# Kernel optimization log

Measured on AMD Instinct MI355X. Metric: run time of the kernel, lower is better.

The kernel has to match this reference:

```python
import jax, jax.numpy as jnp
import numpy as np

B, S, D, H, DFF = 2, 2048, 1024, 16, 4096
DK = D // H
EPS = 1e-6


def layer_norm(x, alpha, bias):
    # TF reduce_std is biased std; eps added to std (not variance)
    mean = jnp.mean(x, axis=-1, keepdims=True)
    std = jnp.sqrt(jnp.mean((x - mean) ** 2, axis=-1, keepdims=True))
    return alpha * (x - mean) / (std + EPS) + bias


def setup_inputs() -> dict:
    key = jax.random.key(0)
    ks = jax.random.split(key, 10)
    s = 0.02
    return {
        "x": jax.random.normal(ks[0], (B, S, D), jnp.float32),
        "mask": jnp.ones((B, 1, 1, S), jnp.int32),
        "wq": jax.random.normal(ks[1], (D, D), jnp.float32) * s,
        "wk": jax.random.normal(ks[2], (D, D), jnp.float32) * s,
        "wv": jax.random.normal(ks[3], (D, D), jnp.float32) * s,
        "wo": jax.random.normal(ks[4], (D, D), jnp.float32) * s,
        "w1": jax.random.normal(ks[5], (D, DFF), jnp.float32) * s,
        "b1": jnp.zeros((DFF,), jnp.float32),
        "w2": jax.random.normal(ks[6], (DFF, D), jnp.float32) * s,
        "b2": jnp.zeros((D,), jnp.float32),
        "ln1_a": jnp.ones((D,), jnp.float32),
        "ln1_b": jnp.zeros((D,), jnp.float32),
        "ln2_a": jnp.ones((D,), jnp.float32),
        "ln2_b": jnp.zeros((D,), jnp.float32),
    }


def reference(x, mask, wq, wk, wv, wo, w1, b1, w2, b2, ln1_a, ln1_b, ln2_a, ln2_b):
    # --- residual 1: pre-norm self-attention ---
    xn = layer_norm(x, ln1_a, ln1_b)
    q = (xn @ wq).reshape(B, S, H, DK)
    k = (xn @ wk).reshape(B, S, H, DK)
    v = (xn @ wv).reshape(B, S, H, DK)
    scores = jnp.einsum('bqhd,bkhd->bhqk', q, k) / jnp.sqrt(jnp.float32(DK))
    scores = jnp.where(mask == 0, jnp.float32(-1e9), scores)
    attn = jax.nn.softmax(scores, axis=-1)  # dropout = identity at eval
    ctx = jnp.einsum('bhqk,bkhd->bqhd', attn, v).reshape(B, S, D)
    x = x + ctx @ wo
    # --- residual 2: pre-norm FFN ---
    xn = layer_norm(x, ln2_a, ln2_b)
    ff = jax.nn.relu(xn @ w1 + b1) @ w2 + b2
    return x + ff
```

## Files before the change

kernel.cpp:

```cpp
#include <hip/hip_runtime.h>

#define BATCH 2
#define SEQ   2048
#define DMODEL 1024
#define NHEAD 16
#define DHEAD 64
#define DFF_  4096
#define MROWS (BATCH*SEQ)
#define EPS 1e-6f

typedef unsigned short u16;
typedef unsigned int u32;
typedef __bf16 bf16x8 __attribute__((ext_vector_type(8)));
typedef float  f32x4  __attribute__((ext_vector_type(4)));
typedef u32    u32x2  __attribute__((ext_vector_type(2)));

__device__ __forceinline__ float bf2f(u16 h) {
    union { u32 u; float f; } v; v.u = ((u32)h) << 16; return v.f;
}
__device__ __forceinline__ u16 f2bf(float f) {
    union { float f; u32 u; } v; v.f = f;
    u32 u = v.u;
    u32 r = (u + 0x7fffu + ((u >> 16) & 1u)) >> 16;
    return (u16)r;
}

__device__ __forceinline__ void async16(const u16* g, u16* l) {
    __builtin_amdgcn_global_load_lds((const __attribute__((address_space(1))) void*)g,
                                     (__attribute__((address_space(3))) void*)l,
                                     16, 0, 0);
}

__global__ __launch_bounds__(256) void transpose_cvt(const float* __restrict__ in,
                                                     u16* __restrict__ out,
                                                     int R, int C) {
    __shared__ float tile[32][33];
    int c0 = blockIdx.x * 32, r0 = blockIdx.y * 32;
    int x = threadIdx.x, y = threadIdx.y;
    #pragma unroll
    for (int i = 0; i < 32; i += 8)
        tile[y + i][x] = in[(size_t)(r0 + y + i) * C + c0 + x];
    __syncthreads();
    #pragma unroll
    for (int i = 0; i < 32; i += 8)
        out[(size_t)(c0 + y + i) * R + r0 + x] = f2bf(tile[x][y + i]);
}

__global__ __launch_bounds__(256) void transpose_v(const u16* __restrict__ qkv,
                                                   u16* __restrict__ vt) {
    __shared__ u16 tile[32][33];
    int bh = blockIdx.z; int b = bh >> 4, h = bh & 15;
    int k0 = blockIdx.x * 32, d0 = blockIdx.y * 32;
    const u16* in = qkv + ((size_t)(b * SEQ)) * 3072 + 2 * DMODEL + h * DHEAD;
    u16* out = vt + ((size_t)bh * DHEAD) * SEQ;
    int x = threadIdx.x, y = threadIdx.y;
    #pragma unroll
    for (int i = 0; i < 32; i += 8)
        tile[y + i][x] = in[(size_t)(k0 + y + i) * 3072 + d0 + x];
    __syncthreads();
    #pragma unroll
    for (int i = 0; i < 32; i += 8)
        out[(size_t)(d0 + y + i) * SEQ + k0 + x] = tile[x][y + i];
}

__global__ __launch_bounds__(256) void ln_kernel(const float* __restrict__ x,
                                                 const float* __restrict__ alpha,
                                                 const float* __restrict__ beta,
                                                 u16* __restrict__ out) {
    int row = blockIdx.x;
    int t = threadIdx.x;
    const float* xr = x + (size_t)row * DMODEL;
    float4 xv = ((const float4*)xr)[t];
    float f0 = xv.x, f1 = xv.y, f2 = xv.z, f3 = xv.w;
    float s1 = f0 + f1 + f2 + f3;
    float s2 = f0*f0 + f1*f1 + f2*f2 + f3*f3;
    #pragma unroll
    for (int off = 32; off >= 1; off >>= 1) {
        s1 += __shfl_xor(s1, off);
        s2 += __shfl_xor(s2, off);
    }
    __shared__ float r1[4], r2[4];
    int w = t >> 6, lane = t & 63;
    if (lane == 0) { r1[w] = s1; r2[w] = s2; }
    __syncthreads();
    s1 = r1[0] + r1[1] + r1[2] + r1[3];
    s2 = r2[0] + r2[1] + r2[2] + r2[3];
    float mean = s1 * (1.0f / DMODEL);
    float var  = s2 * (1.0f / DMODEL) - mean * mean;
    var = fmaxf(var, 0.0f);
    float inv = 1.0f / (sqrtf(var) + EPS);
    float4 av = ((const float4*)alpha)[t];
    float4 bv = ((const float4*)beta)[t];
    ushort4 ov;
    ov.x = f2bf(av.x * (f0 - mean) * inv + bv.x);
    ov.y = f2bf(av.y * (f1 - mean) * inv + bv.y);
    ov.z = f2bf(av.z * (f2 - mean) * inv + bv.z);
    ov.w = f2bf(av.w * (f3 - mean) * inv + bv.w);
    ((ushort4*)(out + (size_t)row * DMODEL))[t] = ov;
}

#define BK 64

template <int AI, int AJ, bool OUT_F32>
__global__ __launch_bounds__(256) void gemm_bt(const u16* __restrict__ A,
                                               const u16* __restrict__ BT,
                                               void* __restrict__ Cp,
                                               const float* __restrict__ bias,
                                               const float* __restrict__ residual,
                                               int M, int N, int K, int do_relu) {
    constexpr int BMt = AI * 32, BNt = AJ * 32;
    __shared__ u16 As[BMt * BK];
    __shared__ u16 Bs[BNt * BK];
    int t = threadIdx.x;
    int m0 = blockIdx.y * BMt, n0 = blockIdx.x * BNt;
    int lane = t & 63, w = t >> 6;
    int wr = w >> 1, wc = w & 1;
    int lhi = lane >> 4, llo = lane & 15;
    int sr = lane >> 3, sk = lane & 7;
    int skx = (sk ^ sr) * 8;

    f32x4 acc[AI][AJ] = {};

    const u16* Ab = A  + (size_t)m0 * K + skx;
    const u16* Bb = BT + (size_t)n0 * K + skx;

    for (int k0 = 0; k0 < K; k0 += BK) {
        __syncthreads();
        #pragma unroll
        for (int j = 0; j < AI; j++) {
            int blk = w * AI + j;
            async16(Ab + (size_t)(blk * 8 + sr) * K + k0, &As[blk * 512]);
        }
        #pragma unroll
        for (int j = 0; j < AJ; j++) {
            int blk = w * AJ + j;
            async16(Bb + (size_t)(blk * 8 + sr) * K + k0, &Bs[blk * 512]);
        }
        __syncthreads();
        #pragma unroll
        for (int kk = 0; kk < 2; kk++) {
            int slot = ((kk * 4 + lhi) ^ (llo & 7)) * 8;
            bf16x8 af[AI], bfr[AJ];
            #pragma unroll
            for (int i = 0; i < AI; i++)
                af[i]  = *(const bf16x8*)(&As[(wr * 16 * AI + i * 16 + llo) * 64 + slot]);
            #pragma unroll
            for (int j = 0; j < AJ; j++)
                bfr[j] = *(const bf16x8*)(&Bs[(wc * 16 * AJ + j * 16 + llo) * 64 + slot]);
            #pragma unroll
            for (int i = 0; i < AI; i++)
                #pragma unroll
                for (int j = 0; j < AJ; j++)
                    acc[i][j] = __builtin_amdgcn_mfma_f32_16x16x32_bf16(af[i], bfr[j], acc[i][j], 0, 0, 0);
        }
    }

    #pragma unroll
    for (int i = 0; i < AI; i++) {
        #pragma unroll
        for (int rr = 0; rr < 4; rr++) {
            int row = m0 + wr * 16 * AI + i * 16 + lhi * 4 + rr;
            #pragma unroll
            for (int j = 0; j < AJ; j++) {
                int col = n0 + wc * 16 * AJ + j * 16 + llo;
                float v = acc[i][j][rr];
                if (bias)      v += bias[col];
                if (residual)  v += residual[(size_t)row * N + col];
                if (do_relu)   v = fmaxf(v, 0.0f);
                size_t idx = (size_t)row * N + col;
                if (OUT_F32) ((float*)Cp)[idx] = v;
                else         ((u16*)Cp)[idx]   = f2bf(v);
            }
        }
    }
}

#define PSTR 68
#define SCL 0.18033688f

__global__ __launch_bounds__(256) void flash_attn(const u16* __restrict__ qkv,
                                                  const u16* __restrict__ vt,
                                                  const int* __restrict__ mask,
                                                  u16* __restrict__ ctx) {
    __shared__ u16 QPs[4 * 16 * PSTR];
    __shared__ u16 Ks[64 * 64];
    __shared__ u16 VTs[64 * 64];
    __shared__ int msk[64];

    int t = threadIdx.x;
    int w = t >> 6, lane = t & 63, lhi = lane >> 4, llo = lane & 15;
    int sr = lane >> 3, sk = lane & 7;
    int skx = (sk ^ sr) * 8;
    int q0 = blockIdx.x * 64, h = blockIdx.y, b = blockIdx.z;

    const u16* Qg  = qkv + ((size_t)(b * SEQ + q0)) * 3072 + h * DHEAD;
    const u16* Kg  = qkv + ((size_t)(b * SEQ)) * 3072 + DMODEL + h * DHEAD;
    const u16* VTg = vt + ((size_t)((b * NHEAD + h) * DHEAD)) * SEQ;

    #pragma unroll
    for (int j = 0; j < 4; j++) {
        int row = (w * 4 + j) * 8 + sr;
        async16(Qg + (size_t)row * 3072 + skx, &QPs[(w * 4 + j) * 512]);
    }
    __syncthreads();
    bf16x8 qf[2];
    #pragma unroll
    for (int kk = 0; kk < 2; kk++)
        qf[kk] = *(const bf16x8*)&QPs[(w * 16 + llo) * 64 + ((kk * 4 + lhi) ^ (llo & 7)) * 8];

    u16* Ps = QPs + w * (16 * PSTR);

    float l_part[4] = {0.0f, 0.0f, 0.0f, 0.0f};
    f32x4 o_acc[4] = {};

    for (int kt = 0; kt < SEQ; kt += 64) {
        __syncthreads();
        #pragma unroll
        for (int j = 0; j < 2; j++) {
            int row = (w * 2 + j) * 8 + sr;
            async16(Kg  + (size_t)(kt + row) * 3072 + skx, &Ks[(w * 2 + j) * 512]);
            async16(VTg + (size_t)row * SEQ + kt + skx,    &VTs[(w * 2 + j) * 512]);
        }
        if (t < 64) msk[t] = mask[b * SEQ + kt + t];
        __syncthreads();

        f32x4 s[4] = {};
        #pragma unroll
        for (int kk = 0; kk < 2; kk++) {
            #pragma unroll
            for (int j = 0; j < 4; j++) {
                bf16x8 kf = *(const bf16x8*)&Ks[(j * 16 + llo) * 64 + ((kk * 4 + lhi) ^ (llo & 7)) * 8];
                s[j] = __builtin_amdgcn_mfma_f32_16x16x32_bf16(qf[kk], kf, s[j], 0, 0, 0);
            }
        }
        #pragma unroll
        for (int j = 0; j < 4; j++) {
            if (msk[j * 16 + llo] == 0) {
                #pragma unroll
                for (int rr = 0; rr < 4; rr++) s[j][rr] = -1.0e13f;
            }
        }
        #pragma unroll
        for (int rr = 0; rr < 4; rr++) {
            #pragma unroll
            for (int j = 0; j < 4; j++) {
                float p = __builtin_amdgcn_exp2f(s[j][rr] * SCL);
                l_part[rr] += p;
                union { float f; u32 u; } pu; pu.f = p;
                Ps[(lhi * 4 + rr) * PSTR + j * 16 + llo] = (u16)(pu.u >> 16);
            }
        }
        #pragma unroll
        for (int kk = 0; kk < 2; kk++) {
            union { bf16x8 v; u32x2 d[2]; } pf;
            const u16* pp = &Ps[llo * PSTR + kk * 32 + lhi * 8];
            pf.d[0] = *(const u32x2*)pp;
            pf.d[1] = *(const u32x2*)(pp + 4);
            #pragma unroll
            for (int nb = 0; nb < 4; nb++) {
                bf16x8 vf = *(const bf16x8*)&VTs[(nb * 16 + llo) * 64 + ((kk * 4 + lhi) ^ (llo & 7)) * 8];
                o_acc[nb] = __builtin_amdgcn_mfma_f32_16x16x32_bf16(pf.v, vf, o_acc[nb], 0, 0, 0);
            }
        }
    }

    #pragma unroll
    for (int rr = 0; rr < 4; rr++) {
        float l = l_part[rr];
        #pragma unroll
        for (int off = 1; off <= 8; off <<= 1) l += __shfl_xor(l, off);
        float inv = __builtin_amdgcn_rcpf(l);
        int row = q0 + w * 16 + lhi * 4 + rr;
        #pragma unroll
        for (int nb = 0; nb < 4; nb++) {
            int col = h * DHEAD + nb * 16 + llo;
            ctx[((size_t)(b * SEQ) + row) * DMODEL + col] = f2bf(o_acc[nb][rr] * inv);
        }
    }
}

extern "C" void kernel_launch(void* const* d_in, const int* in_sizes, int n_in,
                              void* d_out, int out_size, void* d_ws, size_t ws_size,
                              hipStream_t stream) {
    (void)in_sizes; (void)n_in; (void)out_size; (void)ws_size;
    const float* x    = (const float*)d_in[0];
    const int* mask   = (const int*)d_in[1];
    const float* wq   = (const float*)d_in[2];
    const float* wk   = (const float*)d_in[3];
    const float* wv   = (const float*)d_in[4];
    const float* wo   = (const float*)d_in[5];
    const float* w1   = (const float*)d_in[6];
    const float* b1   = (const float*)d_in[7];
    const float* w2   = (const float*)d_in[8];
    const float* b2   = (const float*)d_in[9];
    const float* ln1a = (const float*)d_in[10];
    const float* ln1b = (const float*)d_in[11];
    const float* ln2a = (const float*)d_in[12];
    const float* ln2b = (const float*)d_in[13];
    float* out = (float*)d_out;

    char* wsb = (char*)d_ws;
    const size_t MB = 1024 * 1024;
    u16*   wqkvT = (u16*)(wsb + 0);
    u16*   woT   = (u16*)(wsb + 6 * MB);
    u16*   w1T   = (u16*)(wsb + 8 * MB);
    u16*   w2T   = (u16*)(wsb + 16 * MB);
    u16*   xn    = (u16*)(wsb + 24 * MB);
    float* x2    = (float*)(wsb + 32 * MB);
    u16*   vt    = (u16*)(wsb + 32 * MB);
    u16*   ctx   = (u16*)(wsb + 48 * MB);
    u16*   qkv   = (u16*)(wsb + 56 * MB);
    u16*   ff1   = (u16*)(wsb + 56 * MB);

    dim3 tb(32, 8);
    transpose_cvt<<<dim3(DMODEL/32, DMODEL/32), tb, 0, stream>>>(wq, wqkvT,               DMODEL, DMODEL);
    transpose_cvt<<<dim3(DMODEL/32, DMODEL/32), tb, 0, stream>>>(wk, wqkvT + 1024*1024,   DMODEL, DMODEL);
    transpose_cvt<<<dim3(DMODEL/32, DMODEL/32), tb, 0, stream>>>(wv, wqkvT + 2*1024*1024, DMODEL, DMODEL);
    transpose_cvt<<<dim3(DMODEL/32, DMODEL/32), tb, 0, stream>>>(wo, woT,                 DMODEL, DMODEL);
    transpose_cvt<<<dim3(DFF_/32,  DMODEL/32),  tb, 0, stream>>>(w1, w1T,                 DMODEL, DFF_);
    transpose_cvt<<<dim3(DMODEL/32, DFF_/32),   tb, 0, stream>>>(w2, w2T,                 DFF_, DMODEL);

    ln_kernel<<<MROWS, 256, 0, stream>>>(x, ln1a, ln1b, xn);
    gemm_bt<4,4,false><<<dim3(3072/128, MROWS/128), 256, 0, stream>>>(xn, wqkvT, qkv,
                                                                      nullptr, nullptr,
                                                                      MROWS, 3072, DMODEL, 0);
    transpose_v<<<dim3(SEQ/32, DHEAD/32, BATCH*NHEAD), tb, 0, stream>>>(qkv, vt);
    flash_attn<<<dim3(SEQ / 64, NHEAD, BATCH), 256, 0, stream>>>(qkv, vt, mask, ctx);
    gemm_bt<2,2,true><<<dim3(DMODEL/64, MROWS/64), 256, 0, stream>>>(ctx, woT, x2,
                                                                     nullptr, x,
                                                                     MROWS, DMODEL, DMODEL, 0);
    ln_kernel<<<MROWS, 256, 0, stream>>>(x2, ln2a, ln2b, xn);
    gemm_bt<4,4,false><<<dim3(DFF_/128, MROWS/128), 256, 0, stream>>>(xn, w1T, ff1,
                                                                     b1, nullptr,
                                                                     MROWS, DFF_, DMODEL, 1);
    gemm_bt<2,2,true><<<dim3(DMODEL/64, MROWS/64), 256, 0, stream>>>(ff1, w2T, out,
                                                                    b2, x2,
                                                                    MROWS, DMODEL, DFF_, 0);
}
```

Before: 399.2 us.

## Use two-wave attention blocks with 32 query rows per wave and permuted V layout

Flash attention now runs 128-thread blocks where each wave handles 32 query rows, so every K and V fragment read from LDS feeds two MFMAs. The V transpose kernel writes key positions in a permuted order so each lane can store its four P values as one packed 8-byte LDS write instead of scattered 16-bit stores. Masking becomes an additive bias folded into an FMA before exp2, and the V transpose uses 16-byte vector loads and stores. In exchange, each wave needs more registers and there are fewer waves per block for hiding latency.

```diff
diff --git a/kernel.cpp b/kernel.cpp
--- a/kernel.cpp
+++ b/kernel.cpp
@@ -46,21 +46,33 @@
         out[(size_t)(c0 + y + i) * R + r0 + x] = f2bf(tile[x][y + i]);
 }
 
-__global__ __launch_bounds__(256) void transpose_v(const u16* __restrict__ qkv,
-                                                   u16* __restrict__ vt) {
-    __shared__ u16 tile[32][33];
-    int bh = blockIdx.z; int b = bh >> 4, h = bh & 15;
-    int k0 = blockIdx.x * 32, d0 = blockIdx.y * 32;
-    const u16* in = qkv + ((size_t)(b * SEQ)) * 3072 + 2 * DMODEL + h * DHEAD;
-    u16* out = vt + ((size_t)bh * DHEAD) * SEQ;
-    int x = threadIdx.x, y = threadIdx.y;
-    #pragma unroll
-    for (int i = 0; i < 32; i += 8)
-        tile[y + i][x] = in[(size_t)(k0 + y + i) * 3072 + d0 + x];
+__global__ __launch_bounds__(256) void transpose_v_perm(const u16* __restrict__ qkv,
+                                                        u16* __restrict__ vtp) {
+    __shared__ u16 tile[64][72];
+    int kt = blockIdx.x * 64;
+    int bh = blockIdx.y; int b = bh >> 4, h = bh & 15;
+    const u16* in = qkv + ((size_t)(b * SEQ + kt)) * 3072 + 2 * DMODEL + h * DHEAD;
+    u16* out = vtp + ((size_t)bh * DHEAD) * SEQ;
+    int t = threadIdx.x;
+    int r = t >> 3, c8 = (t & 7) * 8;
+    #pragma unroll
+    for (int pass = 0; pass < 2; pass++) {
+        int row = r + pass * 32;
+        uint4 v = *(const uint4*)(in + (size_t)row * 3072 + c8);
+        *(uint4*)&tile[row][c8] = v;
+    }
     __syncthreads();
     #pragma unroll
-    for (int i = 0; i < 32; i += 8)
-        out[(size_t)(d0 + y + i) * SEQ + k0 + x] = tile[x][y + i];
+    for (int pass = 0; pass < 2; pass++) {
+        int d = r + pass * 32;
+        u16 o8[8];
+        #pragma unroll
+        for (int e = 0; e < 8; e++) {
+            int c = c8 + e;
+            o8[e] = tile[(c & 3) * 16 + (c >> 2)][d];
+        }
+        *(uint4*)(out + (size_t)d * SEQ + kt + c8) = *(const uint4*)o8;
+    }
 }
 
 __global__ __launch_bounds__(256) void ln_kernel(const float* __restrict__ x,
@@ -175,106 +187,120 @@
     }
 }
 
-#define PSTR 68
+#define PSTR 72
 #define SCL 0.18033688f
 
-__global__ __launch_bounds__(256) void flash_attn(const u16* __restrict__ qkv,
-                                                  const u16* __restrict__ vt,
+__global__ __launch_bounds__(128) void flash_attn(const u16* __restrict__ qkv,
+                                                  const u16* __restrict__ vtp,
                                                   const int* __restrict__ mask,
                                                   u16* __restrict__ ctx) {
-    __shared__ u16 QPs[4 * 16 * PSTR];
+    __shared__ u16 QPs[2 * 32 * PSTR];
     __shared__ u16 Ks[64 * 64];
     __shared__ u16 VTs[64 * 64];
-    __shared__ int msk[64];
+    __shared__ float mbias[64];
 
     int t = threadIdx.x;
-    int w = t >> 6, lane = t & 63, lhi = lane >> 4, llo = lane & 15;
+    int wv = t >> 6, lane = t & 63, lhi = lane >> 4, llo = lane & 15;
     int sr = lane >> 3, sk = lane & 7;
     int skx = (sk ^ sr) * 8;
     int q0 = blockIdx.x * 64, h = blockIdx.y, b = blockIdx.z;
 
     const u16* Qg  = qkv + ((size_t)(b * SEQ + q0)) * 3072 + h * DHEAD;
     const u16* Kg  = qkv + ((size_t)(b * SEQ)) * 3072 + DMODEL + h * DHEAD;
-    const u16* VTg = vt + ((size_t)((b * NHEAD + h) * DHEAD)) * SEQ;
+    const u16* VTg = vtp + ((size_t)((b * NHEAD + h) * DHEAD)) * SEQ;
 
     #pragma unroll
     for (int j = 0; j < 4; j++) {
-        int row = (w * 4 + j) * 8 + sr;
-        async16(Qg + (size_t)row * 3072 + skx, &QPs[(w * 4 + j) * 512]);
+        int blk = wv * 4 + j;
+        async16(Qg + (size_t)(blk * 8 + sr) * 3072 + skx, &QPs[blk * 512]);
     }
     __syncthreads();
-    bf16x8 qf[2];
-    #pragma unroll
-    for (int kk = 0; kk < 2; kk++)
-        qf[kk] = *(const bf16x8*)&QPs[(w * 16 + llo) * 64 + ((kk * 4 + lhi) ^ (llo & 7)) * 8];
-
-    u16* Ps = QPs + w * (16 * PSTR);
-
-    float l_part[4] = {0.0f, 0.0f, 0.0f, 0.0f};
-    f32x4 o_acc[4] = {};
+    bf16x8 qf[2][2];
+    #pragma unroll
+    for (int mi = 0; mi < 2; mi++)
+        #pragma unroll
+        for (int kk = 0; kk < 2; kk++)
+            qf[mi][kk] = *(const bf16x8*)&QPs[(wv * 32 + mi * 16 + llo) * 64 +
+                                              ((kk * 4 + lhi) ^ (llo & 7)) * 8];
+
+    u16* Ps = QPs + wv * (32 * PSTR);
+
+    float l_part[2][4] = {};
+    f32x4 o_acc[2][4] = {};
 
     for (int kt = 0; kt < SEQ; kt += 64) {
         __syncthreads();
         #pragma unroll
-        for (int j = 0; j < 2; j++) {
-            int row = (w * 2 + j) * 8 + sr;
-            async16(Kg  + (size_t)(kt + row) * 3072 + skx, &Ks[(w * 2 + j) * 512]);
-            async16(VTg + (size_t)row * SEQ + kt + skx,    &VTs[(w * 2 + j) * 512]);
-        }
-        if (t < 64) msk[t] = mask[b * SEQ + kt + t];
+        for (int j = 0; j < 4; j++) {
+            int blk = wv * 4 + j;
+            async16(Kg  + (size_t)(kt + blk * 8 + sr) * 3072 + skx, &Ks[blk * 512]);
+            async16(VTg + (size_t)(blk * 8 + sr) * SEQ + kt + skx,  &VTs[blk * 512]);
+        }
+        if (t < 64) mbias[t] = (mask[b * SEQ + kt + t] == 0) ? -1.0e12f : 0.0f;
         __syncthreads();
 
-        f32x4 s[4] = {};
+        f32x4 s0[4] = {}, s1[4] = {};
         #pragma unroll
         for (int kk = 0; kk < 2; kk++) {
             #pragma unroll
             for (int j = 0; j < 4; j++) {
-                bf16x8 kf = *(const bf16x8*)&Ks[(j * 16 + llo) * 64 + ((kk * 4 + lhi) ^ (llo & 7)) * 8];
-                s[j] = __builtin_amdgcn_mfma_f32_16x16x32_bf16(qf[kk], kf, s[j], 0, 0, 0);
-            }
-        }
-        #pragma unroll
-        for (int j = 0; j < 4; j++) {
-            if (msk[j * 16 + llo] == 0) {
+                bf16x8 kf = *(const bf16x8*)&Ks[(j * 16 + llo) * 64 +
+                                                ((kk * 4 + lhi) ^ (llo & 7)) * 8];
+                s0[j] = __builtin_amdgcn_mfma_f32_16x16x32_bf16(qf[0][kk], kf, s0[j], 0, 0, 0);
+                s1[j] = __builtin_amdgcn_mfma_f32_16x16x32_bf16(qf[1][kk], kf, s1[j], 0, 0, 0);
+            }
+        }
+        float mb[4];
+        #pragma unroll
+        for (int j = 0; j < 4; j++) mb[j] = mbias[j * 16 + llo];
+
+        #pragma unroll
+        for (int mi = 0; mi < 2; mi++) {
+            const f32x4* s = mi ? s1 : s0;
+            #pragma unroll
+            for (int rr = 0; rr < 4; rr++) {
+                u32 pu[4];
                 #pragma unroll
-                for (int rr = 0; rr < 4; rr++) s[j][rr] = -1.0e13f;
-            }
-        }
+                for (int j = 0; j < 4; j++) {
+                    float p = __builtin_amdgcn_exp2f(__builtin_fmaf(s[j][rr], SCL, mb[j]));
+                    l_part[mi][rr] += p;
+                    union { float f; u32 u; } c; c.f = p;
+                    pu[j] = c.u;
+                }
+                u32x2 w;
+                w[0] = (pu[0] >> 16) | (pu[1] & 0xffff0000u);
+                w[1] = (pu[2] >> 16) | (pu[3] & 0xffff0000u);
+                *(u32x2*)&Ps[(mi * 16 + lhi * 4 + rr) * PSTR + llo * 4] = w;
+            }
+        }
+        #pragma unroll
+        for (int kk = 0; kk < 2; kk++) {
+            bf16x8 pf0 = *(const bf16x8*)&Ps[(0 * 16 + llo) * PSTR + kk * 32 + lhi * 8];
+            bf16x8 pf1 = *(const bf16x8*)&Ps[(1 * 16 + llo) * PSTR + kk * 32 + lhi * 8];
+            #pragma unroll
+            for (int nb = 0; nb < 4; nb++) {
+                bf16x8 vf = *(const bf16x8*)&VTs[(nb * 16 + llo) * 64 +
+                                                 ((kk * 4 + lhi) ^ (llo & 7)) * 8];
+                o_acc[0][nb] = __builtin_amdgcn_mfma_f32_16x16x32_bf16(pf0, vf, o_acc[0][nb], 0, 0, 0);
+                o_acc[1][nb] = __builtin_amdgcn_mfma_f32_16x16x32_bf16(pf1, vf, o_acc[1][nb], 0, 0, 0);
+            }
+        }
+    }
+
+    #pragma unroll
+    for (int mi = 0; mi < 2; mi++) {
         #pragma unroll
         for (int rr = 0; rr < 4; rr++) {
-            #pragma unroll
-            for (int j = 0; j < 4; j++) {
-                float p = __builtin_amdgcn_exp2f(s[j][rr] * SCL);
-                l_part[rr] += p;
-                union { float f; u32 u; } pu; pu.f = p;
-                Ps[(lhi * 4 + rr) * PSTR + j * 16 + llo] = (u16)(pu.u >> 16);
-            }
-        }
-        #pragma unroll
-        for (int kk = 0; kk < 2; kk++) {
-            union { bf16x8 v; u32x2 d[2]; } pf;
-            const u16* pp = &Ps[llo * PSTR + kk * 32 + lhi * 8];
-            pf.d[0] = *(const u32x2*)pp;
-            pf.d[1] = *(const u32x2*)(pp + 4);
+            float l = l_part[mi][rr];
+            #pragma unroll
+            for (int off = 1; off <= 8; off <<= 1) l += __shfl_xor(l, off);
+            float inv = __builtin_amdgcn_rcpf(l);
+            int row = q0 + wv * 32 + mi * 16 + lhi * 4 + rr;
             #pragma unroll
             for (int nb = 0; nb < 4; nb++) {
-                bf16x8 vf = *(const bf16x8*)&VTs[(nb * 16 + llo) * 64 + ((kk * 4 + lhi) ^ (llo & 7)) * 8];
-                o_acc[nb] = __builtin_amdgcn_mfma_f32_16x16x32_bf16(pf.v, vf, o_acc[nb], 0, 0, 0);
-            }
-        }
-    }
-
-    #pragma unroll
-    for (int rr = 0; rr < 4; rr++) {
-        float l = l_part[rr];
-        #pragma unroll
-        for (int off = 1; off <= 8; off <<= 1) l += __shfl_xor(l, off);
-        float inv = __builtin_amdgcn_rcpf(l);
-        int row = q0 + w * 16 + lhi * 4 + rr;
-        #pragma unroll
-        for (int nb = 0; nb < 4; nb++) {
-            int col = h * DHEAD + nb * 16 + llo;
-            ctx[((size_t)(b * SEQ) + row) * DMODEL + col] = f2bf(o_acc[nb][rr] * inv);
+                int col = h * DHEAD + nb * 16 + llo;
+                ctx[((size_t)(b * SEQ) + row) * DMODEL + col] = f2bf(o_acc[mi][nb][rr] * inv);
+            }
         }
     }
 }
@@ -307,7 +333,7 @@
     u16*   w2T   = (u16*)(wsb + 16 * MB);
     u16*   xn    = (u16*)(wsb + 24 * MB);
     float* x2    = (float*)(wsb + 32 * MB);
-    u16*   vt    = (u16*)(wsb + 32 * MB);
+    u16*   vtp   = (u16*)(wsb + 32 * MB);
     u16*   ctx   = (u16*)(wsb + 48 * MB);
     u16*   qkv   = (u16*)(wsb + 56 * MB);
     u16*   ff1   = (u16*)(wsb + 56 * MB);
@@ -324,8 +350,8 @@
     gemm_bt<4,4,false><<<dim3(3072/128, MROWS/128), 256, 0, stream>>>(xn, wqkvT, qkv,
                                                                       nullptr, nullptr,
                                                                       MROWS, 3072, DMODEL, 0);
-    transpose_v<<<dim3(SEQ/32, DHEAD/32, BATCH*NHEAD), tb, 0, stream>>>(qkv, vt);
-    flash_attn<<<dim3(SEQ / 64, NHEAD, BATCH), 256, 0, stream>>>(qkv, vt, mask, ctx);
+    transpose_v_perm<<<dim3(SEQ/64, BATCH*NHEAD), 256, 0, stream>>>(qkv, vtp);
+    flash_attn<<<dim3(SEQ/64, NHEAD, BATCH), 128, 0, stream>>>(qkv, vtp, mask, ctx);
     gemm_bt<2,2,true><<<dim3(DMODEL/64, MROWS/64), 256, 0, stream>>>(ctx, woT, x2,
                                                                      nullptr, x,
                                                                      MROWS, DMODEL, DMODEL, 0);
```

New measurement: 401.1 us. About the same (+0.5%).
